# Performance work log

Hardware: AMD Instinct MI355X
Metric: run time of the kernel (lower is better)

## Reference

```python
import jax, jax.numpy as jnp
import numpy as np
from jax import lax

B, S, V, H, L = 256, 512, 4, 512, 2


def _uniform(key, shape, k):
    return jax.random.uniform(key, shape, dtype=jnp.float32, minval=-k, maxval=k)


def setup_inputs() -> dict:
    key = jax.random.key(0)
    ks = jax.random.split(key, 20)
    ke = 1.0 / np.sqrt(H)   # PyTorch RNN init bound for encoder (hidden=512)
    kd = 1.0 / np.sqrt(V)   # decoder hidden = vocab = 4
    inp = {
        "x": jax.random.normal(ks[0], (B, S, V), dtype=jnp.float32),
        # encoder layer 0: input V -> hidden H
        "e_Wih0": _uniform(ks[1], (H, V), ke),
        "e_Whh0": _uniform(ks[2], (H, H), ke),
        "e_bih0": _uniform(ks[3], (H,), ke),
        "e_bhh0": _uniform(ks[4], (H,), ke),
        # encoder layer 1: H -> H
        "e_Wih1": _uniform(ks[5], (H, H), ke),
        "e_Whh1": _uniform(ks[6], (H, H), ke),
        "e_bih1": _uniform(ks[7], (H,), ke),
        "e_bhh1": _uniform(ks[8], (H,), ke),
        # decoder layer 0: H -> V
        "d_Wih0": _uniform(ks[9], (V, H), kd),
        "d_Whh0": _uniform(ks[10], (V, V), kd),
        "d_bih0": _uniform(ks[11], (V,), kd),
        "d_bhh0": _uniform(ks[12], (V,), kd),
        # decoder layer 1: V -> V
        "d_Wih1": _uniform(ks[13], (V, V), kd),
        "d_Whh1": _uniform(ks[14], (V, V), kd),
        "d_bih1": _uniform(ks[15], (V,), kd),
        "d_bhh1": _uniform(ks[16], (V,), kd),
    }
    return inp


def _rnn_layer(xs, Wih, Whh, bih, bhh):
    # xs: (S, B, in) -> outputs (S, B, hid), final hidden (B, hid)
    h0 = jnp.zeros((xs.shape[1], Whh.shape[0]), dtype=xs.dtype)

    def step(h, xt):
        h = jnp.tanh(xt @ Wih.T + bih + h @ Whh.T + bhh)
        return h, h

    hT, ys = lax.scan(step, h0, xs)
    return ys, hT


def reference(x, e_Wih0, e_Whh0, e_bih0, e_bhh0, e_Wih1, e_Whh1, e_bih1, e_bhh1,
              d_Wih0, d_Whh0, d_bih0, d_bhh0, d_Wih1, d_Whh1, d_bih1, d_bhh1):
    # ---- Encoder: 2-layer tanh RNN over sequence, take last-layer final hidden, atanh ----
    xs = jnp.transpose(x, (1, 0, 2))                     # (S, B, V) time-major
    y1, _ = _rnn_layer(xs, e_Wih0, e_Whh0, e_bih0, e_bhh0)
    _, h2T = _rnn_layer(y1, e_Wih1, e_Whh1, e_bih1, e_bhh1)
    encoded = jnp.arctanh(h2T)[None]                     # (1, B, H)

    # ---- Decoder: softmax(encoded, dim=1) i.e. over BATCH axis (faithful to source) ----
    enc_sm = jax.nn.softmax(encoded, axis=1)[0]          # (B, H)
    a1 = enc_sm @ d_Wih0.T + d_bih0                      # constant per-step input term (B, V)

    h1_0 = jnp.zeros((x.shape[0], d_Whh0.shape[0]), dtype=x.dtype)
    h2_0 = jnp.zeros((x.shape[0], d_Whh1.shape[0]), dtype=x.dtype)

    def dstep(carry, _):
        h1, h2 = carry
        h1 = jnp.tanh(a1 + h1 @ d_Whh0.T + d_bhh0)
        h2 = jnp.tanh(h1 @ d_Wih1.T + d_bih1 + h2 @ d_Whh1.T + d_bhh1)
        return (h1, h2), h2

    _, decodes = lax.scan(dstep, (h1_0, h2_0), None, length=x.shape[1])  # (S, B, V)
    return jnp.transpose(decodes, (1, 0, 2))             # (B, S, V)
```

## Files before the change

kernel.cpp:

```cpp
#include <hip/hip_runtime.h>
#include <hip/hip_bf16.h>

#define NB 256
#define NS 512
#define NV 4
#define NH 512
#define CH 16
#define NCH 32

typedef __bf16 bf16x8 __attribute__((ext_vector_type(8)));
typedef float  f32x4  __attribute__((ext_vector_type(4)));
typedef int    i32x4  __attribute__((ext_vector_type(4)));

#define H1RING_OFF  8192
#define ZRING_OFF   (H1RING_OFF + (4u << 20))
#define ENC_OFF     (ZRING_OFF + (16u << 20))
#define CM_OFF      (ENC_OFF + NB*NH*4)
#define RS_OFF      (CM_OFF + 2048)
#define FRAG_OFF    (RS_OFF + 2048)
#define SCALE_OFF   (FRAG_OFF + 3*262144)

__device__ __forceinline__ float fast_tanh(float x) {
    x = fminf(12.0f, fmaxf(-12.0f, x));
    float e = __expf(2.0f * x);
    return (e - 1.0f) / (e + 1.0f);
}

__device__ __forceinline__ int aload(int* p) {
    return __hip_atomic_load(p, __ATOMIC_ACQUIRE, __HIP_MEMORY_SCOPE_AGENT);
}

__global__ void prep_kernel(const float* __restrict__ W0, const float* __restrict__ W1,
                            const float* __restrict__ WG, char* __restrict__ ws)
{
    const int mt = blockIdx.x >> 5;
    const int gt = blockIdx.x & 31;
    const float* src = (mt == 0) ? W0 : (mt == 1) ? W1 : WG;
    char*  dst = ws + FRAG_OFF + (size_t)mt * 262144;
    float* fsc = (float*)(ws + SCALE_OFF) + mt * 512;
    const int tid = threadIdx.x;
    const int cg = tid >> 4, ti = tid & 15;

    __shared__ float cmax[16][17];
    __shared__ float inv[16];

    {
        const int col = gt * 16 + cg;
        float m = 0.f;
        for (int e = ti; e < NH; e += 16) m = fmaxf(m, fabsf(src[(size_t)col * NH + e]));
        cmax[cg][ti] = m;
    }
    __syncthreads();
    if (ti == 0) {
        float mm = 0.f;
#pragma unroll
        for (int j = 0; j < 16; ++j) mm = fmaxf(mm, cmax[cg][j]);
        inv[cg] = (mm > 0.f) ? 127.0f / mm : 0.f;
        fsc[gt * 16 + cg] = mm / (127.0f * 127.0f);
    }
    __syncthreads();

    for (int e = tid; e < 512; e += 256) {
        const int ks = e >> 6, l = e & 63;
        const int c16 = l & 15;
        const float iv = inv[c16];
        const float* p = src + (size_t)(gt * 16 + c16) * NH + ks * 64 + ((l >> 4) << 4);
        int vi[4];
#pragma unroll
        for (int w = 0; w < 4; ++w) {
            int b0 = __float2int_rn(p[w*4+0] * iv) & 255;
            int b1 = __float2int_rn(p[w*4+1] * iv) & 255;
            int b2 = __float2int_rn(p[w*4+2] * iv) & 255;
            int b3 = __float2int_rn(p[w*4+3] * iv) & 255;
            vi[w] = b0 | (b1 << 8) | (b2 << 16) | (b3 << 24);
        }
        *(i32x4*)(dst + ((size_t)(ks * 32 + gt) * 64 + l) * 16) = (i32x4){vi[0], vi[1], vi[2], vi[3]};
    }
}

extern "C" __global__ __launch_bounds__(512, 1)
void persist_kernel(const float* __restrict__ x,
                    const float* __restrict__ eWih0,
                    const float* __restrict__ ebih0, const float* __restrict__ ebhh0,
                    const float* __restrict__ ebih1, const float* __restrict__ ebhh1,
                    char* __restrict__ ws)
{
    extern __shared__ char lds[];
    int*   F      = (int*)ws;
    char*  h1ring = ws + H1RING_OFF;
    char*  zring  = ws + ZRING_OFF;
    float* enc    = (float*)(ws + ENC_OFF);

    const int blk  = blockIdx.x;
    const int role = blk >> 4;
    const int g    = blk & 15;
    const int tid  = threadIdx.x;
    const int wq   = tid >> 6;
    const int l    = tid & 63;
    const int lm   = l & 15;
    const int q    = l >> 4;

    const int mt = (role == 0) ? 0 : (role == 1) ? 1 : 2;
    const char*  frag = ws + FRAG_OFF + (size_t)mt * 262144;
    const float* fsc  = (const float*)(ws + SCALE_OFF) + mt * 512;

    char* HS = lds;
    char* WL = lds + 16384;

    i32x4 WR[4][4];
#pragma unroll
    for (int ks = 0; ks < 4; ++ks)
#pragma unroll
        for (int n = 0; n < 4; ++n)
            WR[ks][n] = *(const i32x4*)(frag + ((size_t)(ks * 32 + wq * 4 + n) * 64 + l) * 16);
#pragma unroll
    for (int ks = 4; ks < 8; ++ks)
#pragma unroll
        for (int n = 0; n < 4; ++n) {
            const i32x4 v = *(const i32x4*)(frag + ((size_t)(ks * 32 + wq * 4 + n) * 64 + l) * 16);
            *(i32x4*)(WL + (((ks - 4) * 32 + wq * 4 + n) * 64 + l) * 16) = v;
        }
    float f[4];
#pragma unroll
    for (int n = 0; n < 4; ++n) f[n] = fsc[wq * 64 + n * 16 + lm];

    if (role <= 1) {
        const bool isA = (role == 0);

        {
            for (int o = tid; o < 512; o += 512) *(f32x4*)(HS + o * 32) = (f32x4){0.f,0.f,0.f,0.f};
            *(f32x4*)(HS + tid * 32 + 16) = (f32x4){0.f,0.f,0.f,0.f};
        }

        bf16x8 EB[4];
        float  bias[4];
#pragma unroll
        for (int n = 0; n < 4; ++n) {
            const int col = wq * 64 + n * 16 + lm;
#pragma unroll
            for (int j = 0; j < 8; ++j) EB[n][j] = (__bf16)0.f;
            if (isA) {
                if (q == 0) {
                    const float4 w0 = *(const float4*)(eWih0 + (size_t)col * NV);
                    EB[n][0] = (__bf16)w0.x; EB[n][1] = (__bf16)w0.y;
                    EB[n][2] = (__bf16)w0.z; EB[n][3] = (__bf16)w0.w;
                }
                bias[n] = ebih0[col] + ebhh0[col];
            } else {
                bias[n] = 0.f;
            }
        }
        __syncthreads();

#pragma unroll 1
        for (int c = 0; c < NCH; ++c) {
            if (isA) {
                if (c >= 2) {
                    if (tid == 0)
                        while (aload(&F[512 + g * 32 + (c - 2)]) < 1)
                            __builtin_amdgcn_s_sleep(2);
                    __syncthreads();
                }
            } else {
                if (tid == 0)
                    while (aload(&F[512 + g * 32 + c]) < 1)
                        __builtin_amdgcn_s_sleep(2);
                __syncthreads();
                __builtin_amdgcn_fence(__ATOMIC_ACQUIRE, "agent");
            }

            char* rsl = h1ring + (size_t)((g * 2 + (c & 1)) * CH) * 8192;
            char* zsl = zring  + (size_t)((g * 2 + (c & 1)) * CH) * 32768;

            f32x4 zn[4];
            if (!isA) {
#pragma unroll
                for (int n = 0; n < 4; ++n)
                    zn[n] = __builtin_nontemporal_load(
                        (const f32x4*)(zsl + ((wq * 4 + n) * 64 + l) * 16));
            }

#pragma unroll 1
            for (int t = 0; t < CH; ++t) {
                const int i  = c * CH + t;
                const int rb = t & 1;
                const char* hsr = HS + rb * 8192;
                char*       hsw = HS + (rb ^ 1) * 8192;

                i32x4 acc[4];
#pragma unroll
                for (int n = 0; n < 4; ++n) acc[n] = (i32x4){0, 0, 0, 0};
                f32x4 xacc[4];
                bf16x8 xa;
                if (isA) {
#pragma unroll
                    for (int n = 0; n < 4; ++n)
                        xacc[n] = (f32x4){bias[n], bias[n], bias[n], bias[n]};
                    const float4 xv = *(const float4*)(x + ((size_t)(g * 16 + lm) * NS + i) * NV);
#pragma unroll
                    for (int j = 0; j < 8; ++j) xa[j] = (__bf16)0.f;
                    if (q == 0) {
                        xa[0] = (__bf16)xv.x; xa[1] = (__bf16)xv.y;
                        xa[2] = (__bf16)xv.z; xa[3] = (__bf16)xv.w;
                    }
#pragma unroll
                    for (int n = 0; n < 4; ++n)
                        xacc[n] = __builtin_amdgcn_mfma_f32_16x16x32_bf16(xa, EB[n], xacc[n], 0, 0, 0);
                } else {
#pragma unroll
                    for (int n = 0; n < 4; ++n) xacc[n] = zn[n];
                    if (t + 1 < CH) {
#pragma unroll
                        for (int n = 0; n < 4; ++n)
                            zn[n] = __builtin_nontemporal_load(
                                (const f32x4*)(zsl + (size_t)(t + 1) * 32768 +
                                               ((wq * 4 + n) * 64 + l) * 16));
                    }
                }

#pragma unroll
                for (int ks = 0; ks < 4; ++ks) {
                    const i32x4 af = *(const i32x4*)(hsr + ks * 1024 + l * 16);
#pragma unroll
                    for (int n = 0; n < 4; ++n)
                        acc[n] = __builtin_amdgcn_mfma_i32_16x16x64_i8(af, WR[ks][n], acc[n], 0, 0, 0);
                }
#pragma unroll
                for (int ks = 4; ks < 8; ++ks) {
                    const i32x4 af = *(const i32x4*)(hsr + ks * 1024 + l * 16);
#pragma unroll
                    for (int n = 0; n < 4; ++n) {
                        const i32x4 bfr = *(const i32x4*)(WL + (((ks - 4) * 32 + wq * 4 + n) * 64 + l) * 16);
                        acc[n] = __builtin_amdgcn_mfma_i32_16x16x64_i8(af, bfr, acc[n], 0, 0, 0);
                    }
                }

                if (!isA && i == NS - 1) {
#pragma unroll
                    for (int n = 0; n < 4; ++n) {
                        const int col = wq * 64 + n * 16 + lm;
#pragma unroll
                        for (int jr = 0; jr < 4; ++jr)
                            enc[(size_t)(g * 16 + q * 4 + jr) * NH + col] =
                                xacc[n][jr] + (float)acc[n][jr] * f[n];
                    }
                } else {
#pragma unroll
                    for (int n = 0; n < 4; ++n) {
#pragma unroll
                        for (int jr = 0; jr < 4; ++jr) {
                            const float s  = xacc[n][jr] + (float)acc[n][jr] * f[n];
                            const float th = fast_tanh(s);
                            const int slot = (q * 4 + jr) | (n << 4);
                            *(char*)(hsw + wq * 1024 + slot * 16 + lm) =
                                (char)__float2int_rn(th * 127.0f);
                        }
                    }
                }
                __syncthreads();

                if (isA) {
                    const i32x4 v = *(const i32x4*)(hsw + tid * 16);
                    __builtin_nontemporal_store(v, (i32x4*)(rsl + (size_t)t * 8192 + tid * 16));
                }
            }

            __syncthreads();
            if (tid == 0) {
                if (isA)
                    __hip_atomic_store(&F[g * 16], c + 1, __ATOMIC_RELEASE, __HIP_MEMORY_SCOPE_AGENT);
                else
                    __hip_atomic_store(&F[256 + g * 16], c + 1, __ATOMIC_RELEASE, __HIP_MEMORY_SCOPE_AGENT);
            }
        }
    } else {
        float bv[4];
#pragma unroll
        for (int n = 0; n < 4; ++n) {
            const int col = wq * 64 + n * 16 + lm;
            bv[n] = ebih1[col] + ebhh1[col];
        }
        __syncthreads();

#pragma unroll 1
        for (int c = 0; c < NCH; ++c) {
            if (tid == 0) {
                while (aload(&F[g * 16]) < c + 1) __builtin_amdgcn_s_sleep(2);
                if (c >= 2)
                    while (aload(&F[256 + g * 16]) < c - 1) __builtin_amdgcn_s_sleep(2);
            }
            __syncthreads();
            __builtin_amdgcn_fence(__ATOMIC_ACQUIRE, "agent");

            const char* rsl = h1ring + (size_t)((g * 2 + (c & 1)) * CH) * 8192;
            char*       zsl = zring  + (size_t)((g * 2 + (c & 1)) * CH) * 32768;

            *(i32x4*)(HS + tid * 16) =
                __builtin_nontemporal_load((const i32x4*)(rsl + tid * 16));
            __syncthreads();

#pragma unroll 1
            for (int t = 0; t < CH; ++t) {
                const char* bufr = HS + (t & 1) * 8192;
                char*       bufw = HS + ((t + 1) & 1) * 8192;
                i32x4 p0;
                const bool pf = (t + 1 < CH);
                if (pf) p0 = __builtin_nontemporal_load(
                            (const i32x4*)(rsl + (size_t)(t + 1) * 8192 + tid * 16));

                i32x4 acc[4];
#pragma unroll
                for (int n = 0; n < 4; ++n) acc[n] = (i32x4){0, 0, 0, 0};
#pragma unroll
                for (int ks = 0; ks < 4; ++ks) {
                    const i32x4 af = *(const i32x4*)(bufr + ks * 1024 + l * 16);
#pragma unroll
                    for (int n = 0; n < 4; ++n)
                        acc[n] = __builtin_amdgcn_mfma_i32_16x16x64_i8(af, WR[ks][n], acc[n], 0, 0, 0);
                }
#pragma unroll
                for (int ks = 4; ks < 8; ++ks) {
                    const i32x4 af = *(const i32x4*)(bufr + ks * 1024 + l * 16);
#pragma unroll
                    for (int n = 0; n < 4; ++n) {
                        const i32x4 bfr = *(const i32x4*)(WL + (((ks - 4) * 32 + wq * 4 + n) * 64 + l) * 16);
                        acc[n] = __builtin_amdgcn_mfma_i32_16x16x64_i8(af, bfr, acc[n], 0, 0, 0);
                    }
                }
#pragma unroll
                for (int n = 0; n < 4; ++n) {
                    f32x4 zv;
#pragma unroll
                    for (int jr = 0; jr < 4; ++jr) zv[jr] = bv[n] + (float)acc[n][jr] * f[n];
                    __builtin_nontemporal_store(zv,
                        (f32x4*)(zsl + (size_t)t * 32768 + ((wq * 4 + n) * 64 + l) * 16));
                }

                __syncthreads();
                if (pf) *(i32x4*)(bufw + tid * 16) = p0;
                __syncthreads();
            }

            __syncthreads();
            if (tid == 0)
                __hip_atomic_store(&F[512 + g * 32 + c], 1, __ATOMIC_RELEASE, __HIP_MEMORY_SCOPE_AGENT);
        }
    }
}

__global__ void colstats_kernel(const float* __restrict__ encoded,
                                float* __restrict__ colmax,
                                float* __restrict__ rsinv)
{
    const int h = blockIdx.x;
    const int lane = threadIdx.x;
    float v[4];
#pragma unroll
    for (int r = 0; r < 4; ++r) v[r] = encoded[(size_t)(lane + 64 * r) * NH + h];
    float mx = fmaxf(fmaxf(v[0], v[1]), fmaxf(v[2], v[3]));
#pragma unroll
    for (int s = 1; s < 64; s <<= 1) mx = fmaxf(mx, __shfl_xor(mx, s));
    float sum = 0.f;
#pragma unroll
    for (int r = 0; r < 4; ++r) sum += __expf(v[r] - mx);
#pragma unroll
    for (int s = 1; s < 64; s <<= 1) sum += __shfl_xor(sum, s);
    if (lane == 0) { colmax[h] = mx; rsinv[h] = 1.0f / sum; }
}

__global__ void decoder_kernel(
    const float* __restrict__ encoded,
    const float* __restrict__ colmax, const float* __restrict__ rsinv,
    const float* __restrict__ dWih0, const float* __restrict__ dWhh0,
    const float* __restrict__ dbih0, const float* __restrict__ dbhh0,
    const float* __restrict__ dWih1, const float* __restrict__ dWhh1,
    const float* __restrict__ dbih1, const float* __restrict__ dbhh1,
    float* __restrict__ out)
{
    const int b = blockIdx.x * 64 + threadIdx.x;

    float W0[16], Wi[16], W1[16];
#pragma unroll
    for (int e = 0; e < 16; ++e) { W0[e] = dWhh0[e]; Wi[e] = dWih1[e]; W1[e] = dWhh1[e]; }

    float c1[4], c2[4];
#pragma unroll
    for (int j = 0; j < 4; ++j) { c1[j] = dbih0[j] + dbhh0[j]; c2[j] = dbih1[j] + dbhh1[j]; }

    const float* er = encoded + (size_t)b * NH;
#pragma unroll 1
    for (int h = 0; h < NH; h += 4) {
        const float4 ev = *(const float4*)(er + h);
        const float4 cm = *(const float4*)(colmax + h);
        const float4 rs = *(const float4*)(rsinv + h);
        float p0 = __expf(ev.x - cm.x) * rs.x;
        float p1 = __expf(ev.y - cm.y) * rs.y;
        float p2 = __expf(ev.z - cm.z) * rs.z;
        float p3 = __expf(ev.w - cm.w) * rs.w;
#pragma unroll
        for (int j = 0; j < 4; ++j) {
            const float4 w = *(const float4*)(dWih0 + (size_t)j * NH + h);
            c1[j] += p0 * w.x + p1 * w.y + p2 * w.z + p3 * w.w;
        }
    }

    float h1[4] = {0.f, 0.f, 0.f, 0.f};
    float h2[4] = {0.f, 0.f, 0.f, 0.f};
    float* op = out + (size_t)b * NS * NV;

#pragma unroll 1
    for (int t = 0; t < NS; ++t) {
        float n1[4];
#pragma unroll
        for (int j = 0; j < 4; ++j)
            n1[j] = fast_tanh(c1[j] + W0[j*4+0]*h1[0] + W0[j*4+1]*h1[1]
                                    + W0[j*4+2]*h1[2] + W0[j*4+3]*h1[3]);
        float n2[4];
#pragma unroll
        for (int j = 0; j < 4; ++j)
            n2[j] = fast_tanh(c2[j] + Wi[j*4+0]*n1[0] + Wi[j*4+1]*n1[1]
                                    + Wi[j*4+2]*n1[2] + Wi[j*4+3]*n1[3]
                                    + W1[j*4+0]*h2[0] + W1[j*4+1]*h2[1]
                                    + W1[j*4+2]*h2[2] + W1[j*4+3]*h2[3]);
#pragma unroll
        for (int j = 0; j < 4; ++j) { h1[j] = n1[j]; h2[j] = n2[j]; }
        *(float4*)(op + (size_t)t * NV) = make_float4(n2[0], n2[1], n2[2], n2[3]);
    }
}

extern "C" void kernel_launch(void* const* d_in, const int* in_sizes, int n_in,
                              void* d_out, int out_size, void* d_ws, size_t ws_size,
                              hipStream_t stream)
{
    const float* x     = (const float*)d_in[0];
    const float* eWih0 = (const float*)d_in[1];
    const float* eWhh0 = (const float*)d_in[2];
    const float* ebih0 = (const float*)d_in[3];
    const float* ebhh0 = (const float*)d_in[4];
    const float* eWih1 = (const float*)d_in[5];
    const float* eWhh1 = (const float*)d_in[6];
    const float* ebih1 = (const float*)d_in[7];
    const float* ebhh1 = (const float*)d_in[8];
    const float* dWih0 = (const float*)d_in[9];
    const float* dWhh0 = (const float*)d_in[10];
    const float* dbih0 = (const float*)d_in[11];
    const float* dbhh0 = (const float*)d_in[12];
    const float* dWih1 = (const float*)d_in[13];
    const float* dWhh1 = (const float*)d_in[14];
    const float* dbih1 = (const float*)d_in[15];
    const float* dbhh1 = (const float*)d_in[16];

    char*  ws     = (char*)d_ws;
    float* enc    = (float*)(ws + ENC_OFF);
    float* colmax = (float*)(ws + CM_OFF);
    float* rsinv  = (float*)(ws + RS_OFF);

    hipFuncSetAttribute((const void*)persist_kernel,
                        hipFuncAttributeMaxDynamicSharedMemorySize, 147456);

    hipMemsetAsync(d_ws, 0, 4096, stream);

    prep_kernel<<<96, 256, 0, stream>>>(eWhh0, eWhh1, eWih1, ws);

    persist_kernel<<<48, 512, 147456, stream>>>(x, eWih0, ebih0, ebhh0,
                                                ebih1, ebhh1, ws);

    colstats_kernel<<<NH, 64, 0, stream>>>(enc, colmax, rsinv);
    decoder_kernel<<<4, 64, 0, stream>>>(enc, colmax, rsinv,
                                         dWih0, dWhh0, dbih0, dbhh0,
                                         dWih1, dWhh1, dbih1, dbhh1,
                                         (float*)d_out);
}
```

Measured before the change: 1.658 ms.

## Offload layer-0 input projection to producer blocks and software-pipeline LDS fragment loads

Adds a fourth group of 16 blocks that computes the layer-0 input projection plus bias ahead of time. It writes the result as bf16 into a new ring buffer and signals readiness per chunk with flags. The layer-0 recurrence now reads this precomputed term instead of loading x and running bf16 MFMAs each step, which shortens the serial critical path. The int8 MFMA loops in both recurrent roles now prefetch the next A fragment from LDS and raise wave priority with s_setprio. The input-projection role uses a triple-buffered LDS ring so one barrier per step can be dropped. The costs are an extra bf16 rounding of the input term, more launched blocks, more LDS, and another cross-block flag dependency.

```diff
diff --git a/kernel.cpp b/kernel.cpp
--- a/kernel.cpp
+++ b/kernel.cpp
@@ -9,6 +9,7 @@
 #define NCH 32
 
 typedef __bf16 bf16x8 __attribute__((ext_vector_type(8)));
+typedef __bf16 bf16x4 __attribute__((ext_vector_type(4)));
 typedef float  f32x4  __attribute__((ext_vector_type(4)));
 typedef int    i32x4  __attribute__((ext_vector_type(4)));
 
@@ -19,6 +20,7 @@
 #define RS_OFF      (CM_OFF + 2048)
 #define FRAG_OFF    (RS_OFF + 2048)
 #define SCALE_OFF   (FRAG_OFF + 3*262144)
+#define XZRING_OFF  (SCALE_OFF + 8192)
 
 __device__ __forceinline__ float fast_tanh(float x) {
     x = fminf(12.0f, fmaxf(-12.0f, x));
@@ -89,6 +91,7 @@
     int*   F      = (int*)ws;
     char*  h1ring = ws + H1RING_OFF;
     char*  zring  = ws + ZRING_OFF;
+    char*  xzring = ws + XZRING_OFF;
     float* enc    = (float*)(ws + ENC_OFF);
 
     const int blk  = blockIdx.x;
@@ -100,12 +103,66 @@
     const int lm   = l & 15;
     const int q    = l >> 4;
 
-    const int mt = (role == 0) ? 0 : (role == 1) ? 1 : 2;
+    if (role == 3) {
+        bf16x8 EB[4];
+        float  bias[4];
+#pragma unroll
+        for (int n = 0; n < 4; ++n) {
+            const int col = wq * 64 + n * 16 + lm;
+#pragma unroll
+            for (int j = 0; j < 8; ++j) EB[n][j] = (__bf16)0.f;
+            if (q == 0) {
+                const float4 w0 = *(const float4*)(eWih0 + (size_t)col * NV);
+                EB[n][0] = (__bf16)w0.x; EB[n][1] = (__bf16)w0.y;
+                EB[n][2] = (__bf16)w0.z; EB[n][3] = (__bf16)w0.w;
+            }
+            bias[n] = ebih0[col] + ebhh0[col];
+        }
+
+#pragma unroll 1
+        for (int c = 0; c < NCH; ++c) {
+            if (c >= 2) {
+                if (tid == 0)
+                    while (aload(&F[g * 16]) < c - 1) __builtin_amdgcn_s_sleep(2);
+                __syncthreads();
+            }
+            char* xzsl = xzring + (size_t)((g * 2 + (c & 1)) * CH) * 16384;
+
+#pragma unroll 1
+            for (int t = 0; t < CH; ++t) {
+                const int i = c * CH + t;
+                const float4 xv = *(const float4*)(x + ((size_t)(g * 16 + lm) * NS + i) * NV);
+                bf16x8 xa;
+#pragma unroll
+                for (int j = 0; j < 8; ++j) xa[j] = (__bf16)0.f;
+                if (q == 0) {
+                    xa[0] = (__bf16)xv.x; xa[1] = (__bf16)xv.y;
+                    xa[2] = (__bf16)xv.z; xa[3] = (__bf16)xv.w;
+                }
+#pragma unroll
+                for (int n = 0; n < 4; ++n) {
+                    f32x4 a = (f32x4){bias[n], bias[n], bias[n], bias[n]};
+                    a = __builtin_amdgcn_mfma_f32_16x16x32_bf16(xa, EB[n], a, 0, 0, 0);
+                    bf16x4 o;
+#pragma unroll
+                    for (int jr = 0; jr < 4; ++jr) o[jr] = (__bf16)a[jr];
+                    __builtin_nontemporal_store(o,
+                        (bf16x4*)(xzsl + (size_t)t * 16384 + ((wq * 4 + n) * 64 + l) * 8));
+                }
+            }
+            __syncthreads();
+            if (tid == 0)
+                __hip_atomic_store(&F[1024 + g * 32 + c], 1, __ATOMIC_RELEASE, __HIP_MEMORY_SCOPE_AGENT);
+        }
+        return;
+    }
+
+    const int mt = role;
     const char*  frag = ws + FRAG_OFF + (size_t)mt * 262144;
     const float* fsc  = (const float*)(ws + SCALE_OFF) + mt * 512;
 
     char* HS = lds;
-    char* WL = lds + 16384;
+    char* WL = lds + 24576;
 
     i32x4 WR[4][4];
 #pragma unroll
@@ -127,53 +184,39 @@
     if (role <= 1) {
         const bool isA = (role == 0);
 
-        {
-            for (int o = tid; o < 512; o += 512) *(f32x4*)(HS + o * 32) = (f32x4){0.f,0.f,0.f,0.f};
-            *(f32x4*)(HS + tid * 32 + 16) = (f32x4){0.f,0.f,0.f,0.f};
-        }
-
-        bf16x8 EB[4];
-        float  bias[4];
-#pragma unroll
-        for (int n = 0; n < 4; ++n) {
-            const int col = wq * 64 + n * 16 + lm;
-#pragma unroll
-            for (int j = 0; j < 8; ++j) EB[n][j] = (__bf16)0.f;
-            if (isA) {
-                if (q == 0) {
-                    const float4 w0 = *(const float4*)(eWih0 + (size_t)col * NV);
-                    EB[n][0] = (__bf16)w0.x; EB[n][1] = (__bf16)w0.y;
-                    EB[n][2] = (__bf16)w0.z; EB[n][3] = (__bf16)w0.w;
-                }
-                bias[n] = ebih0[col] + ebhh0[col];
-            } else {
-                bias[n] = 0.f;
-            }
-        }
+        *(f32x4*)(HS + tid * 32)      = (f32x4){0.f, 0.f, 0.f, 0.f};
+        *(f32x4*)(HS + tid * 32 + 16) = (f32x4){0.f, 0.f, 0.f, 0.f};
         __syncthreads();
 
 #pragma unroll 1
         for (int c = 0; c < NCH; ++c) {
             if (isA) {
-                if (c >= 2) {
-                    if (tid == 0)
-                        while (aload(&F[512 + g * 32 + (c - 2)]) < 1)
-                            __builtin_amdgcn_s_sleep(2);
-                    __syncthreads();
-                }
+                if (tid == 0) {
+                    while (aload(&F[1024 + g * 32 + c]) < 1) __builtin_amdgcn_s_sleep(2);
+                    if (c >= 2)
+                        while (aload(&F[512 + g * 32 + (c - 2)]) < 1) __builtin_amdgcn_s_sleep(2);
+                }
+                __syncthreads();
+                __builtin_amdgcn_fence(__ATOMIC_ACQUIRE, "agent");
             } else {
                 if (tid == 0)
-                    while (aload(&F[512 + g * 32 + c]) < 1)
-                        __builtin_amdgcn_s_sleep(2);
+                    while (aload(&F[512 + g * 32 + c]) < 1) __builtin_amdgcn_s_sleep(2);
                 __syncthreads();
                 __builtin_amdgcn_fence(__ATOMIC_ACQUIRE, "agent");
             }
 
-            char* rsl = h1ring + (size_t)((g * 2 + (c & 1)) * CH) * 8192;
-            char* zsl = zring  + (size_t)((g * 2 + (c & 1)) * CH) * 32768;
-
-            f32x4 zn[4];
-            if (!isA) {
+            char* rsl  = h1ring + (size_t)((g * 2 + (c & 1)) * CH) * 8192;
+            char* zsl  = zring  + (size_t)((g * 2 + (c & 1)) * CH) * 32768;
+            char* xzsl = xzring + (size_t)((g * 2 + (c & 1)) * CH) * 16384;
+
+            f32x4  zn[4];
+            bf16x4 xzn[4];
+            if (isA) {
+#pragma unroll
+                for (int n = 0; n < 4; ++n)
+                    xzn[n] = __builtin_nontemporal_load(
+                        (const bf16x4*)(xzsl + ((wq * 4 + n) * 64 + l) * 8));
+            } else {
 #pragma unroll
                 for (int n = 0; n < 4; ++n)
                     zn[n] = __builtin_nontemporal_load(
@@ -187,28 +230,23 @@
                 const char* hsr = HS + rb * 8192;
                 char*       hsw = HS + (rb ^ 1) * 8192;
 
-                i32x4 acc[4];
-#pragma unroll
-                for (int n = 0; n < 4; ++n) acc[n] = (i32x4){0, 0, 0, 0};
-                f32x4 xacc[4];
-                bf16x8 xa;
+                f32x4 base[4];
                 if (isA) {
 #pragma unroll
-                    for (int n = 0; n < 4; ++n)
-                        xacc[n] = (f32x4){bias[n], bias[n], bias[n], bias[n]};
-                    const float4 xv = *(const float4*)(x + ((size_t)(g * 16 + lm) * NS + i) * NV);
-#pragma unroll
-                    for (int j = 0; j < 8; ++j) xa[j] = (__bf16)0.f;
-                    if (q == 0) {
-                        xa[0] = (__bf16)xv.x; xa[1] = (__bf16)xv.y;
-                        xa[2] = (__bf16)xv.z; xa[3] = (__bf16)xv.w;
-                    }
-#pragma unroll
-                    for (int n = 0; n < 4; ++n)
-                        xacc[n] = __builtin_amdgcn_mfma_f32_16x16x32_bf16(xa, EB[n], xacc[n], 0, 0, 0);
+                    for (int n = 0; n < 4; ++n) {
+#pragma unroll
+                        for (int jr = 0; jr < 4; ++jr) base[n][jr] = (float)xzn[n][jr];
+                    }
+                    if (t + 1 < CH) {
+#pragma unroll
+                        for (int n = 0; n < 4; ++n)
+                            xzn[n] = __builtin_nontemporal_load(
+                                (const bf16x4*)(xzsl + (size_t)(t + 1) * 16384 +
+                                                ((wq * 4 + n) * 64 + l) * 8));
+                    }
                 } else {
 #pragma unroll
-                    for (int n = 0; n < 4; ++n) xacc[n] = zn[n];
+                    for (int n = 0; n < 4; ++n) base[n] = zn[n];
                     if (t + 1 < CH) {
 #pragma unroll
                         for (int n = 0; n < 4; ++n)
@@ -218,22 +256,30 @@
                     }
                 }
 
-#pragma unroll
-                for (int ks = 0; ks < 4; ++ks) {
-                    const i32x4 af = *(const i32x4*)(hsr + ks * 1024 + l * 16);
-#pragma unroll
-                    for (int n = 0; n < 4; ++n)
-                        acc[n] = __builtin_amdgcn_mfma_i32_16x16x64_i8(af, WR[ks][n], acc[n], 0, 0, 0);
-                }
-#pragma unroll
-                for (int ks = 4; ks < 8; ++ks) {
-                    const i32x4 af = *(const i32x4*)(hsr + ks * 1024 + l * 16);
-#pragma unroll
-                    for (int n = 0; n < 4; ++n) {
-                        const i32x4 bfr = *(const i32x4*)(WL + (((ks - 4) * 32 + wq * 4 + n) * 64 + l) * 16);
-                        acc[n] = __builtin_amdgcn_mfma_i32_16x16x64_i8(af, bfr, acc[n], 0, 0, 0);
-                    }
-                }
+                i32x4 acc[4];
+#pragma unroll
+                for (int n = 0; n < 4; ++n) acc[n] = (i32x4){0, 0, 0, 0};
+
+                __builtin_amdgcn_s_setprio(1);
+                i32x4 afc = *(const i32x4*)(hsr + l * 16);
+#pragma unroll
+                for (int ks = 0; ks < 8; ++ks) {
+                    i32x4 afn;
+                    if (ks < 7) afn = *(const i32x4*)(hsr + (ks + 1) * 1024 + l * 16);
+                    if (ks < 4) {
+#pragma unroll
+                        for (int n = 0; n < 4; ++n)
+                            acc[n] = __builtin_amdgcn_mfma_i32_16x16x64_i8(afc, WR[ks][n], acc[n], 0, 0, 0);
+                    } else {
+#pragma unroll
+                        for (int n = 0; n < 4; ++n) {
+                            const i32x4 bfr = *(const i32x4*)(WL + (((ks - 4) * 32 + wq * 4 + n) * 64 + l) * 16);
+                            acc[n] = __builtin_amdgcn_mfma_i32_16x16x64_i8(afc, bfr, acc[n], 0, 0, 0);
+                        }
+                    }
+                    afc = afn;
+                }
+                __builtin_amdgcn_s_setprio(0);
 
                 if (!isA && i == NS - 1) {
 #pragma unroll
@@ -242,14 +288,14 @@
 #pragma unroll
                         for (int jr = 0; jr < 4; ++jr)
                             enc[(size_t)(g * 16 + q * 4 + jr) * NH + col] =
-                                xacc[n][jr] + (float)acc[n][jr] * f[n];
+                                base[n][jr] + (float)acc[n][jr] * f[n];
                     }
                 } else {
 #pragma unroll
                     for (int n = 0; n < 4; ++n) {
 #pragma unroll
                         for (int jr = 0; jr < 4; ++jr) {
-                            const float s  = xacc[n][jr] + (float)acc[n][jr] * f[n];
+                            const float s  = base[n][jr] + (float)acc[n][jr] * f[n];
                             const float th = fast_tanh(s);
                             const int slot = (q * 4 + jr) | (n << 4);
                             *(char*)(hsw + wq * 1024 + slot * 16 + lm) =
@@ -301,8 +347,8 @@
 
 #pragma unroll 1
             for (int t = 0; t < CH; ++t) {
-                const char* bufr = HS + (t & 1) * 8192;
-                char*       bufw = HS + ((t + 1) & 1) * 8192;
+                const char* bufr = HS + (t % 3) * 8192;
+                char*       bufw = HS + ((t + 1) % 3) * 8192;
                 i32x4 p0;
                 const bool pf = (t + 1 < CH);
                 if (pf) p0 = __builtin_nontemporal_load(
@@ -311,22 +357,28 @@
                 i32x4 acc[4];
 #pragma unroll
                 for (int n = 0; n < 4; ++n) acc[n] = (i32x4){0, 0, 0, 0};
-#pragma unroll
-                for (int ks = 0; ks < 4; ++ks) {
-                    const i32x4 af = *(const i32x4*)(bufr + ks * 1024 + l * 16);
-#pragma unroll
-                    for (int n = 0; n < 4; ++n)
-                        acc[n] = __builtin_amdgcn_mfma_i32_16x16x64_i8(af, WR[ks][n], acc[n], 0, 0, 0);
-                }
-#pragma unroll
-                for (int ks = 4; ks < 8; ++ks) {
-                    const i32x4 af = *(const i32x4*)(bufr + ks * 1024 + l * 16);
-#pragma unroll
-                    for (int n = 0; n < 4; ++n) {
-                        const i32x4 bfr = *(const i32x4*)(WL + (((ks - 4) * 32 + wq * 4 + n) * 64 + l) * 16);
-                        acc[n] = __builtin_amdgcn_mfma_i32_16x16x64_i8(af, bfr, acc[n], 0, 0, 0);
-                    }
-                }
+
+                __builtin_amdgcn_s_setprio(1);
+                i32x4 afc = *(const i32x4*)(bufr + l * 16);
+#pragma unroll
+                for (int ks = 0; ks < 8; ++ks) {
+                    i32x4 afn;
+                    if (ks < 7) afn = *(const i32x4*)(bufr + (ks + 1) * 1024 + l * 16);
+                    if (ks < 4) {
+#pragma unroll
+                        for (int n = 0; n < 4; ++n)
+                            acc[n] = __builtin_amdgcn_mfma_i32_16x16x64_i8(afc, WR[ks][n], acc[n], 0, 0, 0);
+                    } else {
+#pragma unroll
+                        for (int n = 0; n < 4; ++n) {
+                            const i32x4 bfr = *(const i32x4*)(WL + (((ks - 4) * 32 + wq * 4 + n) * 64 + l) * 16);
+                            acc[n] = __builtin_amdgcn_mfma_i32_16x16x64_i8(afc, bfr, acc[n], 0, 0, 0);
+                        }
+                    }
+                    afc = afn;
+                }
+                __builtin_amdgcn_s_setprio(0);
+
 #pragma unroll
                 for (int n = 0; n < 4; ++n) {
                     f32x4 zv;
@@ -336,12 +388,10 @@
                         (f32x4*)(zsl + (size_t)t * 32768 + ((wq * 4 + n) * 64 + l) * 16));
                 }
 
-                __syncthreads();
                 if (pf) *(i32x4*)(bufw + tid * 16) = p0;
                 __syncthreads();
             }
 
-            __syncthreads();
             if (tid == 0)
                 __hip_atomic_store(&F[512 + g * 32 + c], 1, __ATOMIC_RELEASE, __HIP_MEMORY_SCOPE_AGENT);
         }
@@ -456,13 +506,13 @@
     float* rsinv  = (float*)(ws + RS_OFF);
 
     hipFuncSetAttribute((const void*)persist_kernel,
-                        hipFuncAttributeMaxDynamicSharedMemorySize, 147456);
-
-    hipMemsetAsync(d_ws, 0, 4096, stream);
+                        hipFuncAttributeMaxDynamicSharedMemorySize, 155648);
+
+    hipMemsetAsync(d_ws, 0, 8192, stream);
 
     prep_kernel<<<96, 256, 0, stream>>>(eWhh0, eWhh1, eWih1, ws);
 
-    persist_kernel<<<48, 512, 147456, stream>>>(x, eWih0, ebih0, ebhh0,
+    persist_kernel<<<64, 512, 155648, stream>>>(x, eWih0, ebih0, ebhh0,
                                                 ebih1, ebhh1, ws);
 
     colstats_kernel<<<NH, 64, 0, stream>>>(enc, colmax, rsinv);
```

Result: slower. 1.824 ms (+10.1%).
